# Kernel tuning notes

Hardware: AMD Instinct MI355X
Metric: run time of the kernel (lower is better)

The kernel has to match this reference:

```python
import jax, jax.numpy as jnp
import numpy as np

GS = 8        # grid_size
MARGIN = 1.0
LAMBDA = 1.0
BIG = 5.0     # mask penalty added to similarity matrix


def _bilinear(desc, coords):
    # desc: (c,h,w); coords: (n,2) as (y,x) in descriptor pixel space
    c, h, w = desc.shape
    y = jnp.clip(coords[:, 0], 0.0, h - 1.0)
    x = jnp.clip(coords[:, 1], 0.0, w - 1.0)
    y0 = jnp.floor(y); x0 = jnp.floor(x)
    y1 = jnp.minimum(y0 + 1.0, h - 1.0)
    x1 = jnp.minimum(x0 + 1.0, w - 1.0)
    wy = y - y0; wx = x - x0
    y0i = y0.astype(jnp.int32); y1i = y1.astype(jnp.int32)
    x0i = x0.astype(jnp.int32); x1i = x1.astype(jnp.int32)
    v00 = desc[:, y0i, x0i]; v01 = desc[:, y0i, x1i]
    v10 = desc[:, y1i, x0i]; v11 = desc[:, y1i, x1i]
    out = (v00 * (1 - wy) * (1 - wx) + v01 * (1 - wy) * wx
           + v10 * wy * (1 - wx) + v11 * wy * wx)
    return out.T  # (n,c)


def _forward(desc1, desc2, homo12, w_vis_mask1, score2):
    b, cdim, hc, wc = desc1.shape
    flat = hc * wc
    H, W = score2.shape[2], score2.shape[3]
    dt = desc1.dtype

    gy, gx = jnp.meshgrid(jnp.arange(hc, dtype=dt), jnp.arange(wc, dtype=dt), indexing='ij')
    # corner coordinate grid in image pixel space, (x,y) order
    coo1 = jnp.stack([gx * GS, gy * GS], -1).reshape(-1, 2)          # (flat,2)
    homog = jnp.concatenate([coo1, jnp.ones((flat, 1), dt)], -1)     # (flat,3)
    wpts = jnp.einsum('bij,nj->bni', homo12, homog)                  # warp by homography
    w_coo = wpts[..., :2] / (wpts[..., 2:3] + 1e-8)                  # (b,flat,2) (x,y)
    w_coo = w_coo[..., ::-1]                                         # swap to (y,x)

    # sample desc2 at warped coords (descriptor pixel space = image / GS)
    w_desc1 = jax.vmap(_bilinear)(desc2, w_coo / GS)                 # (b,flat,c)

    # center coordinate grid of desc2 cells, (y,x)
    coo2 = jnp.stack([gy * GS + GS / 2, gx * GS + GS / 2], -1).reshape(-1, 2)
    d2 = jnp.sum((w_coo[:, :, None, :] - coo2[None, None, :, :]) ** 2, -1)  # (b,flat,flat)
    ul = jnp.argmin(d2, -1)                                          # (b,flat)
    ur = jnp.where(ul + 1 >= flat, ul, ul + 1)
    ll = jnp.where(ul + wc >= flat, ul, ul + wc)
    lr = jnp.where(ll + 1 >= flat, ll, ll + 1)
    ids = jnp.stack([ul, ur, ll, lr], -1)                            # (b,flat,4)
    bi = jnp.arange(b)[:, None, None]
    ni = jnp.arange(flat)[None, :, None]
    neigh = jnp.zeros((b, flat, flat), dt).at[bi, ni, ids].set(1.0)

    # cell visible only if every pixel in the GSxGS cell is visible
    vis = w_vis_mask1.reshape(b, hc, GS, wc, GS).all(axis=(2, 4)).reshape(b, 1, flat)

    d1f = desc1.reshape(b, cdim, flat).transpose(0, 2, 1)            # (b,flat,c)
    d2f = desc2.reshape(b, cdim, flat).transpose(0, 2, 1)
    sim = 2.0 - 2.0 * jnp.einsum('bnc,bmc->bnm', d1f, d2f)           # inv similarity
    sim = sim + neigh * BIG + (1.0 - vis.astype(dt)) * BIG

    wv = ((w_coo[..., 0] >= 0) & (w_coo[..., 0] < H)
          & (w_coo[..., 1] >= 0) & (w_coo[..., 1] < W)).astype(dt)   # (b,flat)

    pos = 2.0 - 2.0 * jnp.sum(d1f * w_desc1, -1)                     # (b,flat)
    neg = jnp.min(sim, -1)
    l = jnp.maximum(pos - neg + MARGIN, 0.0) ** 2 * wv
    return jnp.sum(l) / jnp.sum(wv) * LAMBDA


def setup_inputs() -> dict:
    key = jax.random.key(0)
    k1, k2, k3, k4, k5 = jax.random.split(key, 5)
    b, c, H, W = 2, 256, 512, 512
    hc, wc = H // GS, W // GS
    d1 = jax.random.normal(k1, (b, c, hc, wc), jnp.float32)
    d1 = d1 / (jnp.linalg.norm(d1, axis=1, keepdims=True) + 1e-8)
    d2 = jax.random.normal(k2, (b, c, hc, wc), jnp.float32)
    d2 = d2 / (jnp.linalg.norm(d2, axis=1, keepdims=True) + 1e-8)
    homo12 = jnp.eye(3, dtype=jnp.float32)[None].repeat(b, 0) \
        + 1e-3 * jax.random.normal(k3, (b, 3, 3), jnp.float32)
    w_vis_mask1 = jax.random.uniform(k4, (b, 1, H, W)) > 0.02
    score2 = jax.random.uniform(k5, (b, 1, H, W), jnp.float32)
    return {"desc1": d1, "desc2": d2, "homo12": homo12,
            "w_vis_mask1": w_vis_mask1, "score2": score2}


def reference(desc1, desc2, homo12, w_vis_mask1, score2):
    return _forward(desc1, desc2, homo12, w_vis_mask1, score2)
```

## Files before the change

### kernel.cpp

```cpp
#include <hip/hip_runtime.h>

typedef __attribute__((ext_vector_type(8))) short s16x8;
typedef __attribute__((ext_vector_type(4))) float f32x4;
typedef __attribute__((ext_vector_type(4))) unsigned short u16x4;

#define FLAT 4096
#define CDIM 256
#define NB 2

#define OFF_D1T  0u
#define OFF_D2T  4194304u
#define OFF_PARTIAL 8388608u
#define OFF_POS  9437184u
#define OFF_WV   9469952u
#define OFF_VIS  9502720u
#define OFF_QUAD 9535488u
#define OFF_RED  9666560u
#define OFF_CNT  9667072u
#define OFF_END  9667328u

__device__ __forceinline__ size_t t16_off(int R, int lane) {
  return (size_t)(R >> 4) * 4096 + ((lane >> 3) * 512) + (((lane >> 1) & 3) * 128) +
         ((R & 15) * 8) + ((lane & 1) * 4);
}

__device__ __forceinline__ float bf2f(unsigned short u) {
  return __uint_as_float(((unsigned)u) << 16);
}
__device__ __forceinline__ unsigned short f2bf(float v) {
  unsigned u = __float_as_uint(v);
  return (unsigned short)((u + 0x7FFFu + ((u >> 16) & 1u)) >> 16);
}
__device__ __forceinline__ void async_g2l(const void* g, void* l) {
  __builtin_amdgcn_global_load_lds(
      (const __attribute__((address_space(1))) unsigned int*)g,
      (__attribute__((address_space(3))) unsigned int*)l,
      16, 0, 0);
}

__global__ __launch_bounds__(256) void k_pre(const float* __restrict__ desc1,
                                             const float* __restrict__ desc2,
                                             unsigned short* __restrict__ d1T,
                                             unsigned short* __restrict__ d2T,
                                             const void* __restrict__ mask,
                                             float* __restrict__ vispen,
                                             unsigned* __restrict__ cnt) {
  __shared__ __align__(16) unsigned ldsw[64 * 128];
  int bid = blockIdx.x;
  int tid = threadIdx.x;
  if (bid < 256) {
    int x = bid & 63, which = (bid >> 6) & 1, b = bid >> 7;
    const float* src = (which ? desc2 : desc1) + (size_t)b * CDIM * FLAT;
    unsigned short* dst = (which ? d2T : d1T) + (size_t)b * FLAT * CDIM;
    int n0 = x * 64;
    int wv = tid >> 6, lane = tid & 63;
    const float* s0 = src + n0 + lane;
#pragma unroll 2
    for (int r = 0; r < 64; r += 8) {
      int c0 = wv * 64 + r;
      float v[8];
#pragma unroll
      for (int t = 0; t < 8; ++t) v[t] = s0[(size_t)(c0 + t) * FLAT];
      unsigned pk[4];
#pragma unroll
      for (int t = 0; t < 4; ++t) pk[t] = (unsigned)f2bf(v[2 * t]) | ((unsigned)f2bf(v[2 * t + 1]) << 16);
      int pg = (c0 >> 3) ^ (lane & 31);
      *(uint4*)(ldsw + lane * 128 + pg * 4) = make_uint4(pk[0], pk[1], pk[2], pk[3]);
    }
    __syncthreads();
    int n = wv * 16 + (lane & 15);
#pragma unroll 2
    for (int it = 0; it < 8; ++it) {
      int g = it * 4 + (lane >> 4);
      uint4 d = *(const uint4*)(ldsw + n * 128 + ((g ^ (n & 31)) * 4));
      *(uint4*)(dst + ((size_t)(n0 >> 4) + wv) * 4096 + it * 512 + lane * 8) = d;
    }
  } else {
    int idx = (bid - 256) * 256 + tid;
    if (idx == 0) *cnt = 0u;
    __shared__ int sflag;
    if (tid < 64) {
      const unsigned* mw = (const unsigned*)mask;
      int odd = 0;
#pragma unroll
      for (int t = 0; t < 16; ++t) {
        unsigned w = mw[tid * 16 + t];
        odd += (w > 1u && w != 0x3F800000u) ? 1 : 0;
      }
#pragma unroll
      for (int d = 32; d >= 1; d >>= 1) odd += __shfl_xor(odd, d, 64);
      if (tid == 0) sflag = (odd > 16) ? 1 : 0;
    }
    __syncthreads();
    int b = idx >> 12, m = idx & 4095;
    int i = m >> 6, j = m & 63;
    bool ok = true;
    if (sflag) {
      const unsigned char* p = (const unsigned char*)mask + (size_t)b * 262144 + (size_t)(i * 8) * 512 + j * 8;
#pragma unroll
      for (int dy = 0; dy < 8; ++dy) {
        const unsigned* q = (const unsigned*)(p + (size_t)dy * 512);
        unsigned w0 = q[0], w1 = q[1];
        unsigned z0 = (w0 - 0x01010101u) & ~w0 & 0x80808080u;
        unsigned z1 = (w1 - 0x01010101u) & ~w1 & 0x80808080u;
        if (z0 | z1) ok = false;
      }
    } else {
      const unsigned* p = (const unsigned*)mask + (size_t)b * 262144 + (size_t)(i * 8) * 512 + j * 8;
#pragma unroll
      for (int dy = 0; dy < 8; ++dy) {
        const uint4* q = (const uint4*)(p + (size_t)dy * 512);
        uint4 u0 = q[0], u1 = q[1];
        if (!(u0.x && u0.y && u0.z && u0.w && u1.x && u1.y && u1.z && u1.w)) ok = false;
      }
    }
    vispen[idx] = ok ? 0.f : 5.f;
  }
}

__global__ void k_setup(const float* __restrict__ homo, const unsigned short* __restrict__ d1T,
                        const unsigned short* __restrict__ d2T, float* __restrict__ pos,
                        float* __restrict__ wv, int4* __restrict__ quads) {
  int b = blockIdx.z;
  int tid = threadIdx.x;
  int wid = tid >> 6, lane = tid & 63;
  int n = blockIdx.x * 4 + wid;
  int i = n >> 6, j = n & 63;
  const float* Hm = homo + b * 9;
  float x = (float)(j * 8), y = (float)(i * 8);
  float den = Hm[6] * x + Hm[7] * y + Hm[8] + 1e-8f;
  float wxc = (Hm[0] * x + Hm[1] * y + Hm[2]) / den;
  float wyc = (Hm[3] * x + Hm[4] * y + Hm[5]) / den;

  float vv = (wyc >= 0.f && wyc < 512.f && wxc >= 0.f && wxc < 512.f) ? 1.f : 0.f;

  int ic = min(63, max(0, (int)floorf(wyc * 0.125f)));
  int jc = min(63, max(0, (int)floorf(wxc * 0.125f)));
  int ul = ic * 64 + jc;
  int ur = (ul + 1 >= FLAT) ? ul : ul + 1;
  int ll = (ul + 64 >= FLAT) ? ul : ul + 64;
  int lr = (ll + 1 >= FLAT) ? ll : ll + 1;

  float cy = fminf(fmaxf(wyc * 0.125f, 0.f), 63.f);
  float cx = fminf(fmaxf(wxc * 0.125f, 0.f), 63.f);
  float y0 = floorf(cy), x0 = floorf(cx);
  float y1 = fminf(y0 + 1.f, 63.f), x1 = fminf(x0 + 1.f, 63.f);
  float fy = cy - y0, fx = cx - x0;
  float w00 = (1.f - fy) * (1.f - fx), w01 = (1.f - fy) * fx;
  float w10 = fy * (1.f - fx), w11 = fy * fx;
  int m00 = (int)y0 * 64 + (int)x0;
  int m01 = (int)y0 * 64 + (int)x1;
  int m10 = (int)y1 * 64 + (int)x0;
  int m11 = (int)y1 * 64 + (int)x1;

  size_t base = (size_t)b * FLAT * CDIM;
  u16x4 a   = *(const u16x4*)(d1T + base + t16_off(n, lane));
  u16x4 v00 = *(const u16x4*)(d2T + base + t16_off(m00, lane));
  u16x4 v01 = *(const u16x4*)(d2T + base + t16_off(m01, lane));
  u16x4 v10 = *(const u16x4*)(d2T + base + t16_off(m10, lane));
  u16x4 v11 = *(const u16x4*)(d2T + base + t16_off(m11, lane));
  float s = 0.f;
#pragma unroll
  for (int t = 0; t < 4; ++t) {
    float vt = w00 * bf2f(v00[t]) + w01 * bf2f(v01[t]) + w10 * bf2f(v10[t]) + w11 * bf2f(v11[t]);
    s += bf2f(a[t]) * vt;
  }
#pragma unroll
  for (int d = 32; d >= 1; d >>= 1) s += __shfl_xor(s, d, 64);
  if (lane == 0) {
    int idx = b * FLAT + n;
    pos[idx] = 2.f - 2.f * s;
    wv[idx] = vv;
    quads[idx] = make_int4(ul, ur, ll, lr);
  }
}

__global__ __launch_bounds__(512, 4) void k_gemm(const unsigned short* __restrict__ d1T,
                                                 const unsigned short* __restrict__ d2T,
                                                 const int4* __restrict__ quads,
                                                 const float* __restrict__ vispen,
                                                 float* __restrict__ partial) {
  __shared__ __align__(16) char lds[3][24576];
  int lin = blockIdx.x;
  int id = (lin & 7) * 128 + (lin >> 3);
  int b = id >> 9;
  int mn = id & 511;
  int m0 = (mn & 31) << 7;
  int n0 = (mn >> 5) << 8;
  int tid = threadIdx.x;
  int wid = tid >> 6, lane = tid & 63;
  int wr = wid >> 1, wc = wid & 1;
  int lg = lane >> 4, ll16 = lane & 15;

  const unsigned short* Ab = d1T + (size_t)b * FLAT * CDIM;
  const unsigned short* Bb = d2T + (size_t)b * FLAT * CDIM;

  const unsigned short* srcq[3];
  int ldsoff[3];
#pragma unroll
  for (int q = 0; q < 3; ++q) {
    int idx = wid * 3 + q;
    int isA = idx < 16;
    int s = isA ? idx : idx - 16;
    int rg = (((isA ? n0 : m0)) >> 4) + s;
    srcq[q] = (isA ? Ab : Bb) + (size_t)rg * 4096 + lane * 8;
    ldsoff[q] = (isA ? 0 : 16384) + s * 1024;
  }

  f32x4 acc[4][4] = {};

#define STAGE(t, p)                                            \
  {                                                            \
    _Pragma("unroll") for (int q = 0; q < 3; ++q)              \
        async_g2l(srcq[q] + (t) * 512, &lds[p][ldsoff[q]]);    \
  }

#define KSTEP(T, WN)                                                                \
  {                                                                                 \
    asm volatile("s_waitcnt vmcnt(" #WN ")" ::: "memory");                          \
    __builtin_amdgcn_s_barrier();                                                   \
    const char* base_ = lds[(T) % 3];                                               \
    s16x8 af[4], bf[4];                                                             \
    _Pragma("unroll") for (int mi = 0; mi < 4; ++mi)                                \
        af[mi] = *(const s16x8*)(base_ + (wr * 4 + mi) * 1024 + lane * 16);         \
    _Pragma("unroll") for (int ni = 0; ni < 4; ++ni)                                \
        bf[ni] = *(const s16x8*)(base_ + 16384 + (wc * 4 + ni) * 1024 + lane * 16); \
    _Pragma("unroll") for (int mi = 0; mi < 4; ++mi)                                \
      _Pragma("unroll") for (int ni = 0; ni < 4; ++ni)                              \
          acc[mi][ni] =                                                             \
              __builtin_amdgcn_mfma_f32_16x16x32_bf16(af[mi], bf[ni], acc[mi][ni], 0, 0, 0); \
    asm volatile("s_waitcnt lgkmcnt(0)" ::: "memory");                              \
    __builtin_amdgcn_s_barrier();                                                   \
    if ((T) < 5) STAGE((T) + 3, ((T) + 3) % 3);                                     \
  }

  STAGE(0, 0);
  STAGE(1, 1);
  STAGE(2, 2);
  KSTEP(0, 6) KSTEP(1, 6) KSTEP(2, 6) KSTEP(3, 6)
  KSTEP(4, 6) KSTEP(5, 6) KSTEP(6, 3) KSTEP(7, 0)
#undef KSTEP
#undef STAGE

  const int4* qB = quads + b * FLAT;
  const float* vB = vispen + b * FLAT;
  float* red = (float*)lds;
  float pv[4];
#pragma unroll
  for (int ni = 0; ni < 4; ++ni) pv[ni] = vB[m0 + wc * 64 + ni * 16 + ll16];
#pragma unroll
  for (int mi = 0; mi < 4; ++mi) {
    int rowBase = wr * 64 + mi * 16 + lg * 4;
    float rm[4] = {1e30f, 1e30f, 1e30f, 1e30f};
    int4 q0 = qB[n0 + rowBase + 0];
    int4 q1 = qB[n0 + rowBase + 1];
    int4 q2 = qB[n0 + rowBase + 2];
    int4 q3 = qB[n0 + rowBase + 3];
#pragma unroll
    for (int ni = 0; ni < 4; ++ni) {
      int gm = m0 + wc * 64 + ni * 16 + ll16;
      f32x4 a = acc[mi][ni];
      float v0 = 2.f - 2.f * a[0] + pv[ni] + ((gm == q0.x || gm == q0.y || gm == q0.z || gm == q0.w) ? 5.f : 0.f);
      float v1 = 2.f - 2.f * a[1] + pv[ni] + ((gm == q1.x || gm == q1.y || gm == q1.z || gm == q1.w) ? 5.f : 0.f);
      float v2 = 2.f - 2.f * a[2] + pv[ni] + ((gm == q2.x || gm == q2.y || gm == q2.z || gm == q2.w) ? 5.f : 0.f);
      float v3 = 2.f - 2.f * a[3] + pv[ni] + ((gm == q3.x || gm == q3.y || gm == q3.z || gm == q3.w) ? 5.f : 0.f);
      rm[0] = fminf(rm[0], v0);
      rm[1] = fminf(rm[1], v1);
      rm[2] = fminf(rm[2], v2);
      rm[3] = fminf(rm[3], v3);
    }
#pragma unroll
    for (int r = 0; r < 4; ++r) {
      float v = rm[r];
#pragma unroll
      for (int d = 1; d < 16; d <<= 1) v = fminf(v, __shfl_xor(v, d, 64));
      if (ll16 == 0) red[(rowBase + r) * 2 + wc] = v;
    }
  }
  __syncthreads();
  if ((wid & 1) == 0) {
    int row = wr * 64 + lane;
    float v = fminf(red[row * 2], red[row * 2 + 1]);
    partial[((size_t)(b * 32 + (m0 >> 7))) * FLAT + n0 + row] = v;
  }
}

__global__ void k_redfin(const float* __restrict__ partial, const float* __restrict__ pos,
                         const float* __restrict__ wv, double* __restrict__ part,
                         unsigned* __restrict__ cnt, float* __restrict__ out) {
  int tid = threadIdx.x;
  int bid = blockIdx.x;
  int idx = bid * 256 + tid;
  int wid = tid >> 6, lane = tid & 63;
  int b = idx >> 12, nl = idx & 4095;
  const float* ps = partial + (size_t)b * 32 * FLAT + nl;
  float neg = 1e30f;
#pragma unroll
  for (int s = 0; s < 32; ++s) neg = fminf(neg, ps[(size_t)s * FLAT]);
  float p = pos[idx], w = wv[idx];
  float t = fmaxf(p - neg + 1.f, 0.f);
  double aL = (double)(t * t) * (double)w;
  double aW = (double)w;
#pragma unroll
  for (int d = 32; d >= 1; d >>= 1) {
    aL += __shfl_xor(aL, d, 64);
    aW += __shfl_xor(aW, d, 64);
  }
  __shared__ double red[8];
  __shared__ int lastFlag;
  if (lane == 0) { red[wid * 2] = aL; red[wid * 2 + 1] = aW; }
  __syncthreads();
  if (tid == 0) {
    double L = 0.0, W = 0.0;
#pragma unroll
    for (int u = 0; u < 4; ++u) { L += red[u * 2]; W += red[u * 2 + 1]; }
    part[bid * 2] = L;
    part[bid * 2 + 1] = W;
    __threadfence();
    unsigned old = atomicAdd(cnt, 1u);
    lastFlag = (old == 31u) ? 1 : 0;
  }
  __syncthreads();
  if (lastFlag && wid == 0) {
    double L = 0.0, W = 0.0;
    if (lane < 32) { L = part[2 * lane]; W = part[2 * lane + 1]; }
#pragma unroll
    for (int d = 16; d >= 1; d >>= 1) {
      L += __shfl_xor(L, d, 64);
      W += __shfl_xor(W, d, 64);
    }
    if (lane == 0) out[0] = (float)(L / W);
  }
}

extern "C" void kernel_launch(void* const* d_in, const int* in_sizes, int n_in,
                              void* d_out, int out_size, void* d_ws, size_t ws_size,
                              hipStream_t stream) {
  if (ws_size < OFF_END) return;
  const float* desc1 = (const float*)d_in[0];
  const float* desc2 = (const float*)d_in[1];
  const float* homo = (const float*)d_in[2];
  const void* mask = d_in[3];

  char* ws = (char*)d_ws;
  unsigned short* d1T = (unsigned short*)(ws + OFF_D1T);
  unsigned short* d2T = (unsigned short*)(ws + OFF_D2T);
  float* partial = (float*)(ws + OFF_PARTIAL);
  float* pos = (float*)(ws + OFF_POS);
  float* wv = (float*)(ws + OFF_WV);
  float* vispen = (float*)(ws + OFF_VIS);
  int4* quads = (int4*)(ws + OFF_QUAD);
  double* part = (double*)(ws + OFF_RED);
  unsigned* cnt = (unsigned*)(ws + OFF_CNT);
  float* out = (float*)d_out;

  k_pre<<<dim3(288), dim3(256), 0, stream>>>(desc1, desc2, d1T, d2T, mask, vispen, cnt);
  k_setup<<<dim3(1024, 1, 2), dim3(256), 0, stream>>>(homo, d1T, d2T, pos, wv, quads);
  k_gemm<<<dim3(1024), dim3(512), 0, stream>>>(d1T, d2T, quads, vispen, partial);
  k_redfin<<<dim3(32), dim3(256), 0, stream>>>(partial, pos, wv, part, cnt, out);
}
```

Baseline: 57.43 us.

## Double-buffer LDS fragment reads to overlap ds_reads with MFMA in GEMM

Restructures the k_gemm main loop to prefetch the next K-step's A/B fragments from LDS into a second register set while MFMAs run on the current set, using a sched_barrier to keep the reads issued first. The vmcnt waits are tightened, and the launch bound is relaxed from 4 to 2 blocks per CU to give the compiler room for the extra fragment registers. The aim is to hide LDS read latency behind matrix math, at the cost of higher register pressure and possibly lower occupancy.

Measured after the change: 62.59 us. 9.0% more time.

```diff
diff --git a/kernel.cpp b/kernel.cpp
--- a/kernel.cpp
+++ b/kernel.cpp
@@ -175,7 +175,7 @@
   }
 }
 
-__global__ __launch_bounds__(512, 4) void k_gemm(const unsigned short* __restrict__ d1T,
+__global__ __launch_bounds__(512, 2) void k_gemm(const unsigned short* __restrict__ d1T,
                                                  const unsigned short* __restrict__ d2T,
                                                  const int4* __restrict__ quads,
                                                  const float* __restrict__ vispen,
@@ -208,6 +208,7 @@
   }
 
   f32x4 acc[4][4] = {};
+  s16x8 a0[4], b0[4], a1[4], b1[4];
 
 #define STAGE(t, p)                                            \
   {                                                            \
@@ -215,31 +216,52 @@
         async_g2l(srcq[q] + (t) * 512, &lds[p][ldsoff[q]]);    \
   }
 
-#define KSTEP(T, WN)                                                                \
+#define DSREAD(BUF, AA, BB)                                                         \
   {                                                                                 \
-    asm volatile("s_waitcnt vmcnt(" #WN ")" ::: "memory");                          \
-    __builtin_amdgcn_s_barrier();                                                   \
-    const char* base_ = lds[(T) % 3];                                               \
-    s16x8 af[4], bf[4];                                                             \
+    const char* base_ = lds[BUF];                                                   \
     _Pragma("unroll") for (int mi = 0; mi < 4; ++mi)                                \
-        af[mi] = *(const s16x8*)(base_ + (wr * 4 + mi) * 1024 + lane * 16);         \
+        AA[mi] = *(const s16x8*)(base_ + (wr * 4 + mi) * 1024 + lane * 16);         \
     _Pragma("unroll") for (int ni = 0; ni < 4; ++ni)                                \
-        bf[ni] = *(const s16x8*)(base_ + 16384 + (wc * 4 + ni) * 1024 + lane * 16); \
+        BB[ni] = *(const s16x8*)(base_ + 16384 + (wc * 4 + ni) * 1024 + lane * 16); \
+  }
+
+#define MFMABLK(AA, BB)                                                             \
+  {                                                                                 \
     _Pragma("unroll") for (int mi = 0; mi < 4; ++mi)                                \
       _Pragma("unroll") for (int ni = 0; ni < 4; ++ni)                              \
           acc[mi][ni] =                                                             \
-              __builtin_amdgcn_mfma_f32_16x16x32_bf16(af[mi], bf[ni], acc[mi][ni], 0, 0, 0); \
-    asm volatile("s_waitcnt lgkmcnt(0)" ::: "memory");                              \
-    __builtin_amdgcn_s_barrier();                                                   \
-    if ((T) < 5) STAGE((T) + 3, ((T) + 3) % 3);                                     \
+              __builtin_amdgcn_mfma_f32_16x16x32_bf16(AA[mi], BB[ni], acc[mi][ni], 0, 0, 0); \
+  }
+
+#define KSTEP(T, WN, CA, CB, NA, NB)                  \
+  {                                                   \
+    asm volatile("s_waitcnt vmcnt(" #WN ")" ::: "memory"); \
+    __builtin_amdgcn_s_barrier();                     \
+    DSREAD(((T) + 1) % 3, NA, NB);                    \
+    __builtin_amdgcn_sched_barrier(0);                \
+    MFMABLK(CA, CB);                                  \
+    __builtin_amdgcn_s_barrier();                     \
+    if ((T) < 5) STAGE((T) + 3, (T) % 3);             \
   }
 
   STAGE(0, 0);
   STAGE(1, 1);
   STAGE(2, 2);
-  KSTEP(0, 6) KSTEP(1, 6) KSTEP(2, 6) KSTEP(3, 6)
-  KSTEP(4, 6) KSTEP(5, 6) KSTEP(6, 3) KSTEP(7, 0)
+  asm volatile("s_waitcnt vmcnt(6)" ::: "memory");
+  __builtin_amdgcn_s_barrier();
+  DSREAD(0, a0, b0);
+  KSTEP(0, 3, a0, b0, a1, b1)
+  KSTEP(1, 3, a1, b1, a0, b0)
+  KSTEP(2, 3, a0, b0, a1, b1)
+  KSTEP(3, 3, a1, b1, a0, b0)
+  KSTEP(4, 3, a0, b0, a1, b1)
+  KSTEP(5, 3, a1, b1, a0, b0)
+  KSTEP(6, 0, a0, b0, a1, b1)
+  MFMABLK(a1, b1)
+  __builtin_amdgcn_s_barrier();
 #undef KSTEP
+#undef MFMABLK
+#undef DSREAD
 #undef STAGE
 
   const int4* qB = quads + b * FLAT;
```

## Enlarge GEMM tile to 256x256 with double-buffered LDS and MFMA priority

Applied to the files above, without the earlier changes.

The similarity GEMM tile grows from 256x128 to 256x256, with 8 waves arranged 2x4 and each wave holding an 8x4 accumulator block. The LDS pipeline moves from triple to double buffering, and the MFMA block is wrapped in setprio and a sched_barrier. This halves the grid to 512 blocks and the partial-min slices from 32 to 16, and k_redfin is updated to match. The goal is more reuse per loaded byte and fewer partials to reduce. The cost is higher register pressure (128 accumulator floats per lane), less prefetch depth, and fewer blocks to fill the CUs.

Result: slower. 192.5 us (+235.1%).

```diff
diff --git a/kernel.cpp b/kernel.cpp
--- a/kernel.cpp
+++ b/kernel.cpp
@@ -180,65 +180,65 @@
                                                  const int4* __restrict__ quads,
                                                  const float* __restrict__ vispen,
                                                  float* __restrict__ partial) {
-  __shared__ __align__(16) char lds[3][24576];
+  __shared__ __align__(16) char lds[65536];
   int lin = blockIdx.x;
-  int id = (lin & 7) * 128 + (lin >> 3);
-  int b = id >> 9;
-  int mn = id & 511;
-  int m0 = (mn & 31) << 7;
-  int n0 = (mn >> 5) << 8;
+  int id = (lin & 7) * 64 + (lin >> 3);
+  int b = id >> 8;
+  int rem = id & 255;
+  int m0 = (rem & 15) << 8;
+  int n0 = (rem >> 4) << 8;
   int tid = threadIdx.x;
   int wid = tid >> 6, lane = tid & 63;
-  int wr = wid >> 1, wc = wid & 1;
+  int wr = wid >> 2, wc = wid & 3;
   int lg = lane >> 4, ll16 = lane & 15;
 
   const unsigned short* Ab = d1T + (size_t)b * FLAT * CDIM;
   const unsigned short* Bb = d2T + (size_t)b * FLAT * CDIM;
 
-  const unsigned short* srcq[3];
-  int ldsoff[3];
-#pragma unroll
-  for (int q = 0; q < 3; ++q) {
-    int idx = wid * 3 + q;
-    int isA = idx < 16;
-    int s = isA ? idx : idx - 16;
-    int rg = (((isA ? n0 : m0)) >> 4) + s;
-    srcq[q] = (isA ? Ab : Bb) + (size_t)rg * 4096 + lane * 8;
-    ldsoff[q] = (isA ? 0 : 16384) + s * 1024;
-  }
-
-  f32x4 acc[4][4] = {};
-
-#define STAGE(t, p)                                            \
-  {                                                            \
-    _Pragma("unroll") for (int q = 0; q < 3; ++q)              \
-        async_g2l(srcq[q] + (t) * 512, &lds[p][ldsoff[q]]);    \
-  }
-
-#define KSTEP(T, WN)                                                                \
-  {                                                                                 \
-    asm volatile("s_waitcnt vmcnt(" #WN ")" ::: "memory");                          \
-    __builtin_amdgcn_s_barrier();                                                   \
-    const char* base_ = lds[(T) % 3];                                               \
-    s16x8 af[4], bf[4];                                                             \
-    _Pragma("unroll") for (int mi = 0; mi < 4; ++mi)                                \
-        af[mi] = *(const s16x8*)(base_ + (wr * 4 + mi) * 1024 + lane * 16);         \
-    _Pragma("unroll") for (int ni = 0; ni < 4; ++ni)                                \
-        bf[ni] = *(const s16x8*)(base_ + 16384 + (wc * 4 + ni) * 1024 + lane * 16); \
-    _Pragma("unroll") for (int mi = 0; mi < 4; ++mi)                                \
-      _Pragma("unroll") for (int ni = 0; ni < 4; ++ni)                              \
-          acc[mi][ni] =                                                             \
-              __builtin_amdgcn_mfma_f32_16x16x32_bf16(af[mi], bf[ni], acc[mi][ni], 0, 0, 0); \
-    asm volatile("s_waitcnt lgkmcnt(0)" ::: "memory");                              \
-    __builtin_amdgcn_s_barrier();                                                   \
-    if ((T) < 5) STAGE((T) + 3, ((T) + 3) % 3);                                     \
-  }
-
-  STAGE(0, 0);
-  STAGE(1, 1);
-  STAGE(2, 2);
-  KSTEP(0, 6) KSTEP(1, 6) KSTEP(2, 6) KSTEP(3, 6)
-  KSTEP(4, 6) KSTEP(5, 6) KSTEP(6, 3) KSTEP(7, 0)
+  const unsigned short* srcq[4];
+  int ldsoff[4];
+#pragma unroll
+  for (int q = 0; q < 4; ++q) {
+    int unit = wid * 4 + q;
+    int isA = unit < 16;
+    int rg = unit & 15;
+    int rgG = ((isA ? n0 : m0) >> 4) + rg;
+    srcq[q] = (isA ? Ab : Bb) + (size_t)rgG * 4096 + lane * 8;
+    ldsoff[q] = (isA ? 0 : 16384) + rg * 1024;
+  }
+
+  f32x4 acc[8][4] = {};
+
+#define STAGE(t)                                                       \
+  { _Pragma("unroll") for (int q = 0; q < 4; ++q)                      \
+      async_g2l(srcq[q] + (t) * 512, &lds[((t) & 1) * 32768 + ldsoff[q]]); }
+
+#define KSTEP(T, WN)                                                              \
+  {                                                                               \
+    asm volatile("s_waitcnt vmcnt(" #WN ")" ::: "memory");                        \
+    __builtin_amdgcn_s_barrier();                                                 \
+    const char* base_ = &lds[((T) & 1) * 32768];                                  \
+    s16x8 af[8]; s16x8 bf[4];                                                     \
+    _Pragma("unroll") for (int i = 0; i < 8; ++i)                                 \
+        af[i] = *(const s16x8*)(base_ + (wr * 8 + i) * 1024 + lane * 16);         \
+    _Pragma("unroll") for (int j = 0; j < 4; ++j)                                 \
+        bf[j] = *(const s16x8*)(base_ + 16384 + (wc * 4 + j) * 1024 + lane * 16); \
+    asm volatile("s_waitcnt lgkmcnt(0)" ::: "memory");                            \
+    __builtin_amdgcn_sched_barrier(0);                                            \
+    __builtin_amdgcn_s_setprio(1);                                                \
+    _Pragma("unroll") for (int i = 0; i < 8; ++i)                                 \
+      _Pragma("unroll") for (int j = 0; j < 4; ++j)                               \
+          acc[i][j] =                                                             \
+              __builtin_amdgcn_mfma_f32_16x16x32_bf16(af[i], bf[j], acc[i][j], 0, 0, 0); \
+    __builtin_amdgcn_s_setprio(0);                                                \
+    __builtin_amdgcn_s_barrier();                                                 \
+    if ((T) < 6) STAGE((T) + 2);                                                  \
+  }
+
+  STAGE(0);
+  STAGE(1);
+  KSTEP(0, 4) KSTEP(1, 4) KSTEP(2, 4) KSTEP(3, 4)
+  KSTEP(4, 4) KSTEP(5, 4) KSTEP(6, 4) KSTEP(7, 0)
 #undef KSTEP
 #undef STAGE
 
@@ -247,23 +247,23 @@
   float* red = (float*)lds;
   float pv[4];
 #pragma unroll
-  for (int ni = 0; ni < 4; ++ni) pv[ni] = vB[m0 + wc * 64 + ni * 16 + ll16];
-#pragma unroll
-  for (int mi = 0; mi < 4; ++mi) {
-    int rowBase = wr * 64 + mi * 16 + lg * 4;
+  for (int j = 0; j < 4; ++j) pv[j] = vB[m0 + wc * 64 + j * 16 + ll16];
+#pragma unroll
+  for (int i = 0; i < 8; ++i) {
+    int rowBase = wr * 128 + i * 16 + lg * 4;
     float rm[4] = {1e30f, 1e30f, 1e30f, 1e30f};
     int4 q0 = qB[n0 + rowBase + 0];
     int4 q1 = qB[n0 + rowBase + 1];
     int4 q2 = qB[n0 + rowBase + 2];
     int4 q3 = qB[n0 + rowBase + 3];
 #pragma unroll
-    for (int ni = 0; ni < 4; ++ni) {
-      int gm = m0 + wc * 64 + ni * 16 + ll16;
-      f32x4 a = acc[mi][ni];
-      float v0 = 2.f - 2.f * a[0] + pv[ni] + ((gm == q0.x || gm == q0.y || gm == q0.z || gm == q0.w) ? 5.f : 0.f);
-      float v1 = 2.f - 2.f * a[1] + pv[ni] + ((gm == q1.x || gm == q1.y || gm == q1.z || gm == q1.w) ? 5.f : 0.f);
-      float v2 = 2.f - 2.f * a[2] + pv[ni] + ((gm == q2.x || gm == q2.y || gm == q2.z || gm == q2.w) ? 5.f : 0.f);
-      float v3 = 2.f - 2.f * a[3] + pv[ni] + ((gm == q3.x || gm == q3.y || gm == q3.z || gm == q3.w) ? 5.f : 0.f);
+    for (int j = 0; j < 4; ++j) {
+      int gm = m0 + wc * 64 + j * 16 + ll16;
+      f32x4 a = acc[i][j];
+      float v0 = 2.f - 2.f * a[0] + pv[j] + ((gm == q0.x || gm == q0.y || gm == q0.z || gm == q0.w) ? 5.f : 0.f);
+      float v1 = 2.f - 2.f * a[1] + pv[j] + ((gm == q1.x || gm == q1.y || gm == q1.z || gm == q1.w) ? 5.f : 0.f);
+      float v2 = 2.f - 2.f * a[2] + pv[j] + ((gm == q2.x || gm == q2.y || gm == q2.z || gm == q2.w) ? 5.f : 0.f);
+      float v3 = 2.f - 2.f * a[3] + pv[j] + ((gm == q3.x || gm == q3.y || gm == q3.z || gm == q3.w) ? 5.f : 0.f);
       rm[0] = fminf(rm[0], v0);
       rm[1] = fminf(rm[1], v1);
       rm[2] = fminf(rm[2], v2);
@@ -274,14 +274,15 @@
       float v = rm[r];
 #pragma unroll
       for (int d = 1; d < 16; d <<= 1) v = fminf(v, __shfl_xor(v, d, 64));
-      if (ll16 == 0) red[(rowBase + r) * 2 + wc] = v;
+      if (ll16 == 0) red[(rowBase + r) * 4 + wc] = v;
     }
   }
   __syncthreads();
-  if ((wid & 1) == 0) {
-    int row = wr * 64 + lane;
-    float v = fminf(red[row * 2], red[row * 2 + 1]);
-    partial[((size_t)(b * 32 + (m0 >> 7))) * FLAT + n0 + row] = v;
+  if (wid < 4) {
+    int row = wid * 64 + lane;
+    float v = fminf(fminf(red[row * 4], red[row * 4 + 1]),
+                    fminf(red[row * 4 + 2], red[row * 4 + 3]));
+    partial[((size_t)(b * 16 + (m0 >> 8))) * FLAT + n0 + row] = v;
   }
 }
 
@@ -293,10 +294,10 @@
   int idx = bid * 256 + tid;
   int wid = tid >> 6, lane = tid & 63;
   int b = idx >> 12, nl = idx & 4095;
-  const float* ps = partial + (size_t)b * 32 * FLAT + nl;
+  const float* ps = partial + (size_t)b * 16 * FLAT + nl;
   float neg = 1e30f;
 #pragma unroll
-  for (int s = 0; s < 32; ++s) neg = fminf(neg, ps[(size_t)s * FLAT]);
+  for (int s = 0; s < 16; ++s) neg = fminf(neg, ps[(size_t)s * FLAT]);
   float p = pos[idx], w = wv[idx];
   float t = fmaxf(p - neg + 1.f, 0.f);
   double aL = (double)(t * t) * (double)w;
@@ -356,6 +357,6 @@
 
   k_pre<<<dim3(288), dim3(256), 0, stream>>>(desc1, desc2, d1T, d2T, mask, vispen, cnt);
   k_setup<<<dim3(1024, 1, 2), dim3(256), 0, stream>>>(homo, d1T, d2T, pos, wv, quads);
-  k_gemm<<<dim3(1024), dim3(512), 0, stream>>>(d1T, d2T, quads, vispen, partial);
+  k_gemm<<<dim3(512), dim3(512), 0, stream>>>(d1T, d2T, quads, vispen, partial);
   k_redfin<<<dim3(32), dim3(256), 0, stream>>>(partial, pos, wv, part, cnt, out);
 }
```

## Fold setup kernel into pre and gemm kernels, add MFMA priority hints

Applied to the files above, without the earlier changes.

Removes the separate k_setup launch. The homography quad-index computation moves into an extra block of k_pre, and the positive-pair bilinear dot products move into 32 extra blocks appended to the k_gemm grid. This is meant to save one kernel launch and its serialization gap. It also raises wave priority around the MFMA loop with s_setprio and makes LDS buffer indices explicit constants. The extra k_gemm blocks add a tail of non-GEMM work that may land after the GEMM blocks.

Measured after the change: 77.64 us. 35.2% more time.

```diff
diff --git a/kernel.cpp b/kernel.cpp
--- a/kernel.cpp
+++ b/kernel.cpp
@@ -44,6 +44,8 @@
                                              unsigned short* __restrict__ d2T,
                                              const void* __restrict__ mask,
                                              float* __restrict__ vispen,
+                                             int4* __restrict__ quads,
+                                             const float* __restrict__ homo,
                                              unsigned* __restrict__ cnt) {
   __shared__ __align__(16) unsigned ldsw[64 * 128];
   int bid = blockIdx.x;
@@ -75,9 +77,27 @@
       uint4 d = *(const uint4*)(ldsw + n * 128 + ((g ^ (n & 31)) * 4));
       *(uint4*)(dst + ((size_t)(n0 >> 4) + wv) * 4096 + it * 512 + lane * 8) = d;
     }
+  } else if (bid == 256) {
+    if (tid == 0) *cnt = 0u;
+    for (int it = 0; it < 32; ++it) {
+      int idx = it * 256 + tid;
+      int b = idx >> 12, n = idx & 4095;
+      int i = n >> 6, j = n & 63;
+      const float* Hm = homo + b * 9;
+      float x = (float)(j * 8), y = (float)(i * 8);
+      float den = Hm[6] * x + Hm[7] * y + Hm[8] + 1e-8f;
+      float wxc = (Hm[0] * x + Hm[1] * y + Hm[2]) / den;
+      float wyc = (Hm[3] * x + Hm[4] * y + Hm[5]) / den;
+      int ic = min(63, max(0, (int)floorf(wyc * 0.125f)));
+      int jc = min(63, max(0, (int)floorf(wxc * 0.125f)));
+      int ul = ic * 64 + jc;
+      int ur = (ul + 1 >= FLAT) ? ul : ul + 1;
+      int ll = (ul + 64 >= FLAT) ? ul : ul + 64;
+      int lr = (ll + 1 >= FLAT) ? ll : ll + 1;
+      quads[idx] = make_int4(ul, ur, ll, lr);
+    }
   } else {
-    int idx = (bid - 256) * 256 + tid;
-    if (idx == 0) *cnt = 0u;
+    int idx = (bid - 257) * 256 + tid;
     __shared__ int sflag;
     if (tid < 64) {
       const unsigned* mw = (const unsigned*)mask;
@@ -118,77 +138,69 @@
   }
 }
 
-__global__ void k_setup(const float* __restrict__ homo, const unsigned short* __restrict__ d1T,
-                        const unsigned short* __restrict__ d2T, float* __restrict__ pos,
-                        float* __restrict__ wv, int4* __restrict__ quads) {
-  int b = blockIdx.z;
-  int tid = threadIdx.x;
-  int wid = tid >> 6, lane = tid & 63;
-  int n = blockIdx.x * 4 + wid;
-  int i = n >> 6, j = n & 63;
-  const float* Hm = homo + b * 9;
-  float x = (float)(j * 8), y = (float)(i * 8);
-  float den = Hm[6] * x + Hm[7] * y + Hm[8] + 1e-8f;
-  float wxc = (Hm[0] * x + Hm[1] * y + Hm[2]) / den;
-  float wyc = (Hm[3] * x + Hm[4] * y + Hm[5]) / den;
-
-  float vv = (wyc >= 0.f && wyc < 512.f && wxc >= 0.f && wxc < 512.f) ? 1.f : 0.f;
-
-  int ic = min(63, max(0, (int)floorf(wyc * 0.125f)));
-  int jc = min(63, max(0, (int)floorf(wxc * 0.125f)));
-  int ul = ic * 64 + jc;
-  int ur = (ul + 1 >= FLAT) ? ul : ul + 1;
-  int ll = (ul + 64 >= FLAT) ? ul : ul + 64;
-  int lr = (ll + 1 >= FLAT) ? ll : ll + 1;
-
-  float cy = fminf(fmaxf(wyc * 0.125f, 0.f), 63.f);
-  float cx = fminf(fmaxf(wxc * 0.125f, 0.f), 63.f);
-  float y0 = floorf(cy), x0 = floorf(cx);
-  float y1 = fminf(y0 + 1.f, 63.f), x1 = fminf(x0 + 1.f, 63.f);
-  float fy = cy - y0, fx = cx - x0;
-  float w00 = (1.f - fy) * (1.f - fx), w01 = (1.f - fy) * fx;
-  float w10 = fy * (1.f - fx), w11 = fy * fx;
-  int m00 = (int)y0 * 64 + (int)x0;
-  int m01 = (int)y0 * 64 + (int)x1;
-  int m10 = (int)y1 * 64 + (int)x0;
-  int m11 = (int)y1 * 64 + (int)x1;
-
-  size_t base = (size_t)b * FLAT * CDIM;
-  u16x4 a   = *(const u16x4*)(d1T + base + t16_off(n, lane));
-  u16x4 v00 = *(const u16x4*)(d2T + base + t16_off(m00, lane));
-  u16x4 v01 = *(const u16x4*)(d2T + base + t16_off(m01, lane));
-  u16x4 v10 = *(const u16x4*)(d2T + base + t16_off(m10, lane));
-  u16x4 v11 = *(const u16x4*)(d2T + base + t16_off(m11, lane));
-  float s = 0.f;
-#pragma unroll
-  for (int t = 0; t < 4; ++t) {
-    float vt = w00 * bf2f(v00[t]) + w01 * bf2f(v01[t]) + w10 * bf2f(v10[t]) + w11 * bf2f(v11[t]);
-    s += bf2f(a[t]) * vt;
-  }
-#pragma unroll
-  for (int d = 32; d >= 1; d >>= 1) s += __shfl_xor(s, d, 64);
-  if (lane == 0) {
-    int idx = b * FLAT + n;
-    pos[idx] = 2.f - 2.f * s;
-    wv[idx] = vv;
-    quads[idx] = make_int4(ul, ur, ll, lr);
-  }
-}
-
 __global__ __launch_bounds__(512, 4) void k_gemm(const unsigned short* __restrict__ d1T,
                                                  const unsigned short* __restrict__ d2T,
                                                  const int4* __restrict__ quads,
                                                  const float* __restrict__ vispen,
+                                                 const float* __restrict__ homo,
+                                                 float* __restrict__ pos,
+                                                 float* __restrict__ wv,
                                                  float* __restrict__ partial) {
   __shared__ __align__(16) char lds[3][24576];
   int lin = blockIdx.x;
+  int tid = threadIdx.x;
+  int wid = tid >> 6, lane = tid & 63;
+
+  if (lin >= 1024) {
+    int sb = lin - 1024;
+    for (int it = 0; it < 32; ++it) {
+      int grow = sb * 256 + wid * 32 + it;
+      int b2 = grow >> 12, n = grow & 4095;
+      int i = n >> 6, j = n & 63;
+      const float* Hm = homo + b2 * 9;
+      float x = (float)(j * 8), y = (float)(i * 8);
+      float den = Hm[6] * x + Hm[7] * y + Hm[8] + 1e-8f;
+      float wxc = (Hm[0] * x + Hm[1] * y + Hm[2]) / den;
+      float wyc = (Hm[3] * x + Hm[4] * y + Hm[5]) / den;
+      float vv = (wyc >= 0.f && wyc < 512.f && wxc >= 0.f && wxc < 512.f) ? 1.f : 0.f;
+      float cy = fminf(fmaxf(wyc * 0.125f, 0.f), 63.f);
+      float cx = fminf(fmaxf(wxc * 0.125f, 0.f), 63.f);
+      float y0 = floorf(cy), x0 = floorf(cx);
+      float y1 = fminf(y0 + 1.f, 63.f), x1 = fminf(x0 + 1.f, 63.f);
+      float fy = cy - y0, fx = cx - x0;
+      float w00 = (1.f - fy) * (1.f - fx), w01 = (1.f - fy) * fx;
+      float w10 = fy * (1.f - fx), w11 = fy * fx;
+      int m00 = (int)y0 * 64 + (int)x0;
+      int m01 = (int)y0 * 64 + (int)x1;
+      int m10 = (int)y1 * 64 + (int)x0;
+      int m11 = (int)y1 * 64 + (int)x1;
+      size_t base = (size_t)b2 * FLAT * CDIM;
+      u16x4 a   = *(const u16x4*)(d1T + base + t16_off(n, lane));
+      u16x4 v00 = *(const u16x4*)(d2T + base + t16_off(m00, lane));
+      u16x4 v01 = *(const u16x4*)(d2T + base + t16_off(m01, lane));
+      u16x4 v10 = *(const u16x4*)(d2T + base + t16_off(m10, lane));
+      u16x4 v11 = *(const u16x4*)(d2T + base + t16_off(m11, lane));
+      float s = 0.f;
+#pragma unroll
+      for (int t = 0; t < 4; ++t) {
+        float vt = w00 * bf2f(v00[t]) + w01 * bf2f(v01[t]) + w10 * bf2f(v10[t]) + w11 * bf2f(v11[t]);
+        s += bf2f(a[t]) * vt;
+      }
+#pragma unroll
+      for (int d = 32; d >= 1; d >>= 1) s += __shfl_xor(s, d, 64);
+      if (lane == 0) {
+        pos[grow] = 2.f - 2.f * s;
+        wv[grow] = vv;
+      }
+    }
+    return;
+  }
+
   int id = (lin & 7) * 128 + (lin >> 3);
   int b = id >> 9;
   int mn = id & 511;
   int m0 = (mn & 31) << 7;
   int n0 = (mn >> 5) << 8;
-  int tid = threadIdx.x;
-  int wid = tid >> 6, lane = tid & 63;
   int wr = wid >> 1, wc = wid & 1;
   int lg = lane >> 4, ll16 = lane & 15;
 
@@ -215,30 +227,32 @@
         async_g2l(srcq[q] + (t) * 512, &lds[p][ldsoff[q]]);    \
   }
 
-#define KSTEP(T, WN)                                                                \
-  {                                                                                 \
-    asm volatile("s_waitcnt vmcnt(" #WN ")" ::: "memory");                          \
-    __builtin_amdgcn_s_barrier();                                                   \
-    const char* base_ = lds[(T) % 3];                                               \
-    s16x8 af[4], bf[4];                                                             \
-    _Pragma("unroll") for (int mi = 0; mi < 4; ++mi)                                \
-        af[mi] = *(const s16x8*)(base_ + (wr * 4 + mi) * 1024 + lane * 16);         \
-    _Pragma("unroll") for (int ni = 0; ni < 4; ++ni)                                \
-        bf[ni] = *(const s16x8*)(base_ + 16384 + (wc * 4 + ni) * 1024 + lane * 16); \
-    _Pragma("unroll") for (int mi = 0; mi < 4; ++mi)                                \
-      _Pragma("unroll") for (int ni = 0; ni < 4; ++ni)                              \
-          acc[mi][ni] =                                                             \
+#define KSTEP(T, BUF, WN)                                                          \
+  {                                                                                \
+    asm volatile("s_waitcnt vmcnt(" #WN ")" ::: "memory");                         \
+    __builtin_amdgcn_s_barrier();                                                  \
+    const char* base_ = lds[BUF];                                                  \
+    s16x8 af[4], bf[4];                                                            \
+    _Pragma("unroll") for (int mi = 0; mi < 4; ++mi)                               \
+        af[mi] = *(const s16x8*)(base_ + (wr * 4 + mi) * 1024 + lane * 16);        \
+    _Pragma("unroll") for (int ni = 0; ni < 4; ++ni)                               \
+        bf[ni] = *(const s16x8*)(base_ + 16384 + (wc * 4 + ni) * 1024 + lane * 16);\
+    __builtin_amdgcn_s_setprio(1);                                                 \
+    _Pragma("unroll") for (int mi = 0; mi < 4; ++mi)                               \
+      _Pragma("unroll") for (int ni = 0; ni < 4; ++ni)                             \
+          acc[mi][ni] =                                                            \
               __builtin_amdgcn_mfma_f32_16x16x32_bf16(af[mi], bf[ni], acc[mi][ni], 0, 0, 0); \
-    asm volatile("s_waitcnt lgkmcnt(0)" ::: "memory");                              \
-    __builtin_amdgcn_s_barrier();                                                   \
-    if ((T) < 5) STAGE((T) + 3, ((T) + 3) % 3);                                     \
+    __builtin_amdgcn_s_setprio(0);                                                 \
+    asm volatile("s_waitcnt lgkmcnt(0)" ::: "memory");                             \
+    __builtin_amdgcn_s_barrier();                                                  \
+    if ((T) < 5) STAGE((T) + 3, ((T) + 3) % 3);                                    \
   }
 
   STAGE(0, 0);
   STAGE(1, 1);
   STAGE(2, 2);
-  KSTEP(0, 6) KSTEP(1, 6) KSTEP(2, 6) KSTEP(3, 6)
-  KSTEP(4, 6) KSTEP(5, 6) KSTEP(6, 3) KSTEP(7, 0)
+  KSTEP(0, 0, 6) KSTEP(1, 1, 6) KSTEP(2, 2, 6) KSTEP(3, 0, 6)
+  KSTEP(4, 1, 6) KSTEP(5, 2, 6) KSTEP(6, 0, 3) KSTEP(7, 1, 0)
 #undef KSTEP
 #undef STAGE
 
@@ -354,8 +368,7 @@
   unsigned* cnt = (unsigned*)(ws + OFF_CNT);
   float* out = (float*)d_out;
 
-  k_pre<<<dim3(288), dim3(256), 0, stream>>>(desc1, desc2, d1T, d2T, mask, vispen, cnt);
-  k_setup<<<dim3(1024, 1, 2), dim3(256), 0, stream>>>(homo, d1T, d2T, pos, wv, quads);
-  k_gemm<<<dim3(1024), dim3(512), 0, stream>>>(d1T, d2T, quads, vispen, partial);
+  k_pre<<<dim3(289), dim3(256), 0, stream>>>(desc1, desc2, d1T, d2T, mask, vispen, quads, homo, cnt);
+  k_gemm<<<dim3(1056), dim3(512), 0, stream>>>(d1T, d2T, quads, vispen, homo, pos, wv, partial);
   k_redfin<<<dim3(32), dim3(256), 0, stream>>>(partial, pos, wv, part, cnt, out);
 }
```
